# Kernel optimization log

Hardware: AMD Instinct MI355X
Metric: run time of the kernel (lower is better)

The kernel has to match this reference:

```python
import jax, jax.numpy as jnp
import numpy as np
from jax import lax

# ---- fake-quant helpers (brevitas-style per-tensor float scaling, STE round) ----
EPS = 1e-8

def _ste_round(x):
    return x + lax.stop_gradient(jnp.round(x) - x)

def _scale(x, qmax):
    s = lax.stop_gradient(jnp.max(jnp.abs(x))) / qmax
    return jnp.maximum(s, EPS)

def fq(x, scale, qmin, qmax):
    # fake-quantize: round-to-nearest with straight-through estimator, clip, dequant
    return jnp.clip(_ste_round(x / scale), qmin, qmax) * scale

def quant_act_int8(x):
    s = _scale(x, 127.0)
    return fq(x, s, -128.0, 127.0), s

def quant_weight_int4(w):
    # 4-bit signed, narrow range [-7, 7] (brevitas weight quant default narrow_range)
    s = _scale(w, 7.0)
    return fq(w, s, -7.0, 7.0), s

def quant_relu_uint4(x):
    y = jax.nn.relu(x)
    s = _scale(y, 15.0)
    return fq(y, s, 0.0, 15.0)

def quant_bias_int32(b, scale):
    # Int32Bias: bias quantized at input_scale * weight_scale
    return _ste_round(b / scale) * scale

def conv2d_same(x, w):
    # NCHW, OIHW, padding=1, stride=1
    return lax.conv_general_dilated(x, w, window_strides=(1, 1), padding=((1, 1), (1, 1)),
                                    dimension_numbers=('NCHW', 'OIHW', 'NCHW'))

def maxpool2(x):
    return lax.reduce_window(x, -jnp.inf, lax.max, (1, 1, 2, 2), (1, 1, 2, 2), 'VALID')

def quant_conv(x, w, b):
    xq, sx = quant_act_int8(x)        # input_quant: Int8ActPerTensorFloat
    wq, sw = quant_weight_int4(w)     # weight_bit_width=4
    bq = quant_bias_int32(b, sx * sw) # bias_quant: Int32Bias
    y = conv2d_same(xq, wq) + bq[None, :, None, None]
    yq, _ = quant_act_int8(y)         # output_quant: Int8ActPerTensorFloat
    return yq

def quant_linear(x, w, b):
    xq, sx = quant_act_int8(x)
    wq, sw = quant_weight_int4(w)
    bq = quant_bias_int32(b, sx * sw)
    y = xq @ wq.T + bq
    yq, _ = quant_act_int8(y)
    return yq


def setup_inputs() -> dict:
    key = jax.random.key(0)
    ks = jax.random.split(key, 7)
    B = 8192
    x = jax.random.normal(ks[0], (B, 1, 28, 28), dtype=jnp.float32)
    w1 = jax.random.normal(ks[1], (16, 1, 3, 3), dtype=jnp.float32) * 0.3
    b1 = jax.random.normal(ks[2], (16,), dtype=jnp.float32) * 0.1
    w2 = jax.random.normal(ks[3], (32, 16, 3, 3), dtype=jnp.float32) * 0.1
    b2 = jax.random.normal(ks[4], (32,), dtype=jnp.float32) * 0.1
    wf = jax.random.normal(ks[5], (10, 32 * 7 * 7), dtype=jnp.float32) * 0.05
    bf = jax.random.normal(ks[6], (10,), dtype=jnp.float32) * 0.1
    return {'x': x, 'w1': w1, 'b1': b1, 'w2': w2, 'b2': b2, 'wf': wf, 'bf': bf}


def reference(x, w1, b1, w2, b2, wf, bf):
    h, _ = quant_act_int8(x)              # inputQuant
    h = quant_conv(h, w1, b1)             # conv1
    h = quant_relu_uint4(h)               # relu1 (4-bit)
    h = maxpool2(h)                       # pool1 -> [B,16,14,14]
    h = quant_conv(h, w2, b2)             # conv2
    h = quant_relu_uint4(h)               # relu2
    h = maxpool2(h)                       # pool2 -> [B,32,7,7]
    h = h.reshape(h.shape[0], -1)         # flatten -> [B,1568]
    return quant_linear(h, wf, bf)        # fc -> [B,10]
```

## Files before the change

### kernel.cpp

```cpp
#include <hip/hip_runtime.h>
#include <climits>

#define NB 8192
#define EPSQ 1e-8f

using i32x4  = __attribute__((ext_vector_type(4)))  int;
using i32x16 = __attribute__((ext_vector_type(16))) int;

#define WS_F(ws)     ((float*)(ws))
#define WS_I(ws)     ((int*)((char*)(ws)+128))
#define WS_B1L(ws)   ((int*)((char*)(ws)+384))
#define WS_B2L(ws)   ((int*)((char*)(ws)+448))
#define WS_BFL(ws)   ((int*)((char*)(ws)+576))
#define WS_M1F(ws)   ((float*)((char*)(ws)+640))
#define WS_B1F(ws)   ((float*)((char*)(ws)+1280))
#define WS_B2FR(ws)  ((char*)(ws)+2048)
#define WS_Q2TAB(ws) ((signed char*)((char*)(ws)+7168))
#define WS_Q3TAB(ws) ((signed char*)((char*)(ws)+7424))
#define WS_B1FR(ws)  ((char*)(ws)+7680)
#define WS_MFF(ws)   ((float*)((char*)(ws)+20480))
#define WS_WFP(ws)   ((char*)(ws)+83200)
#define WS_RA1(ws)   ((int*)((char*)(ws)+139264))
#define WS_RS1(ws)   ((int*)((char*)(ws)+164352))
#define WS_RA2(ws)   ((int*)((char*)(ws)+189440))
#define WS_RS2(ws)   ((int*)((char*)(ws)+197632))
#define WS_RA3(ws)   ((int*)((char*)(ws)+205824))
#define WS_RAX(ws)   ((float*)((char*)(ws)+206848))
#define WS_WMX(ws)   ((float*)((char*)(ws)+215040))
#define WS_Q2B(ws)   ((signed char*)((char*)(ws)+215552))
#define WS_BIG_OFF   281600

__device__ __forceinline__ float clampf(float v, float lo, float hi){ return fminf(fmaxf(v, lo), hi); }

__device__ __forceinline__ float wave_max_f(float v){
#pragma unroll
  for (int off=32; off; off>>=1) v = fmaxf(v, __shfl_down(v, off, 64));
  return v;
}
__device__ __forceinline__ int wave_max_i(int v){
#pragma unroll
  for (int off=32; off; off>>=1) v = max(v, __shfl_down(v, off, 64));
  return v;
}

__device__ __forceinline__ void reduce2_atomic(int amax, int smax, int* gA, int* gS){
  amax = wave_max_i(amax); smax = wave_max_i(smax);
  __shared__ int sA[4], sS[4];
  int w = threadIdx.x>>6, l = threadIdx.x&63;
  if (l==0){ sA[w]=amax; sS[w]=smax; }
  __syncthreads();
  if (threadIdx.x==0){
#pragma unroll
    for (int i=1;i<4;i++){ amax=max(amax,sA[i]); smax=max(smax,sS[i]); }
    atomicMax(gA, amax); atomicMax(gS, smax);
  }
}

__device__ __forceinline__ void reduce2_store(int amax, int smax, int* pA, int* pS){
  amax = wave_max_i(amax); smax = wave_max_i(smax);
  __shared__ int sA[4], sS[4];
  int w = threadIdx.x>>6, l = threadIdx.x&63;
  if (l==0){ sA[w]=amax; sS[w]=smax; }
  __syncthreads();
  if (threadIdx.x==0){
#pragma unroll
    for (int i=1;i<4;i++){ amax=max(amax,sA[i]); smax=max(smax,sS[i]); }
    *pA = amax; *pS = smax;
  }
}

__global__ void k_init(char* ws){
  int* I = WS_I(ws);
  if (threadIdx.x==0){ I[0]=0; I[1]=0; I[2]=INT_MIN; I[3]=0; I[4]=INT_MIN; I[5]=0; }
}

__global__ void k_absx(const float* __restrict__ x, char* ws){
  const float4* x4 = (const float4*)x;
  const int n4 = NB*784/4;
  float m = 0.f;
  for (int i = blockIdx.x*blockDim.x + threadIdx.x; i < n4; i += gridDim.x*blockDim.x){
    float4 v = x4[i];
    m = fmaxf(m, fmaxf(fmaxf(fabsf(v.x),fabsf(v.y)), fmaxf(fabsf(v.z),fabsf(v.w))));
  }
  m = wave_max_f(m);
  __shared__ float sm[4];
  int w = threadIdx.x>>6;
  if ((threadIdx.x&63)==0) sm[w]=m;
  __syncthreads();
  if (threadIdx.x==0){
    m = fmaxf(fmaxf(sm[0],sm[1]), fmaxf(sm[2],sm[3]));
    WS_RAX(ws)[blockIdx.x] = m;
  }
}

__global__ void k_wmax(const float* __restrict__ w1, const float* __restrict__ w2,
                       const float* __restrict__ wf, char* ws){
  __shared__ float red[256];
  int b = blockIdx.x, t = threadIdx.x;
  float m = 0.f;
  if (b==0){ if (t<144) m = fabsf(w1[t]); }
  else if (b<19){ m = fabsf(w2[(b-1)*256 + t]); }
  else { int i=(b-19)*256+t; if (i<15680) m = fabsf(wf[i]); }
  red[t]=m; __syncthreads();
  for (int s=128;s;s>>=1){ if (t<s) red[t]=fmaxf(red[t],red[t+s]); __syncthreads(); }
  if (t==0) WS_WMX(ws)[b]=red[0];
}

__global__ void k_scales(const float* __restrict__ w1, const float* __restrict__ b1, char* ws){
  __shared__ float red[256];
  float* F = WS_F(ws);
  int t = threadIdx.x;
  float vw1 = WS_WMX(ws)[0];
  float m2=0.f, mf=0.f;
  if (t<18) m2 = WS_WMX(ws)[1+t];
  if (t<62) mf = WS_WMX(ws)[19+t];
  red[t]=m2; __syncthreads();
  for (int s=128;s;s>>=1){ if (t<s) red[t]=fmaxf(red[t],red[t+s]); __syncthreads(); }
  float mw2=red[0]; __syncthreads();
  red[t]=mf; __syncthreads();
  for (int s=128;s;s>>=1){ if (t<s) red[t]=fmaxf(red[t],red[t+s]); __syncthreads(); }
  float mwf=red[0]; __syncthreads();
  float mxv=0.f;
  for (int i=t;i<2048;i+=256) mxv=fmaxf(mxv,WS_RAX(ws)[i]);
  red[t]=mxv; __syncthreads();
  for (int s=128;s;s>>=1){ if (t<s) red[t]=fmaxf(red[t],red[t+s]); __syncthreads(); }
  float mx=red[0]; __syncthreads();

  float s0  = fmaxf(mx/127.f, EPSQ);
  float sx1 = fmaxf((127.f*s0)/127.f, EPSQ);
  float sw1 = fmaxf(vw1/7.f, EPSQ);
  float sw2 = fmaxf(mw2/7.f, EPSQ);
  float swf = fmaxf(mwf/7.f, EPSQ);
  float sb1 = sx1*sw1;
  if (t==0){ F[0]=s0; F[1]=sx1; F[2]=sw1; F[3]=sb1; F[7]=sw2; F[12]=swf; }
  if (t<144) WS_M1F(ws)[t] = clampf(rintf(w1[t]/sw1), -7.f, 7.f);
  if (t<16){
    int bl = (int)rintf(b1[t]/sb1);
    WS_B1L(ws)[t] = bl;
    WS_B1F(ws)[t] = (float)bl;
  }
}

__global__ void k_pack(const float* __restrict__ w1, const float* __restrict__ w2,
                       const float* __restrict__ wf, char* ws){
  const float* F = WS_F(ws);
  int id = blockIdx.x*256 + threadIdx.x;
  if (id < 5120){
    float sw2 = F[7];
    int chunk=id>>10, r=id&1023, ln=r>>4, j=r&15;
    int tap=2*chunk+(ln>>5), oc=ln&31;
    signed char v=0;
    if (tap<9) v=(signed char)clampf(rintf(w2[oc*144 + j*9 + tap]/sw2), -7.f, 7.f);
    WS_B2FR(ws)[id]=v;
  } else if (id < 6144){
    float sw1 = F[2];
    int i=id-5120;
    int ln=i>>4, j=i&15;
    int k=(ln>>5)*16+j, oc=ln&31;
    signed char v=0;
    if (k<9 && oc<16) v=(signed char)clampf(rintf(w1[oc*9+k]/sw1), -7.f, 7.f);
    WS_B1FR(ws)[i]=v;
  } else if (id < 56320){
    float swf = F[12];
    int i=id-6144;
    int chunk=i>>10, r2=i&1023, ln=r2>>4, j=r2&15;
    int oc=ln&31, k=chunk*32+(ln>>5)*16+j;
    int cell=k>>5, ch=k&31;
    signed char v=0;
    if (oc<10) v=(signed char)clampf(rintf(wf[oc*1568 + ch*49 + cell]/swf), -7.f, 7.f);
    ((signed char*)WS_WFP(ws))[i]=v;
  } else if (id < 72000){
    float swf = F[12];
    int i=id-56320;
    WS_MFF(ws)[i] = clampf(rintf(wf[i]/swf), -7.f, 7.f);
  }
}

__global__ void k_wq(const float* __restrict__ w1, const float* __restrict__ b1,
                     const float* __restrict__ w2, const float* __restrict__ wf,
                     char* ws){
  __shared__ float red[256];
  float* F = WS_F(ws);
  int t = threadIdx.x;
  auto bmaxabs = [&](const float* p, int n)->float{
    float m=0.f; for (int i=t;i<n;i+=256) m=fmaxf(m,fabsf(p[i]));
    red[t]=m; __syncthreads();
    for (int s=128;s;s>>=1){ if (t<s) red[t]=fmaxf(red[t],red[t+s]); __syncthreads(); }
    float r=red[0]; __syncthreads(); return r;
  };
  float mw1 = bmaxabs(w1,144);
  float mw2 = bmaxabs(w2,4608);
  float mwf = bmaxabs(wf,15680);
  float mxv=0.f;
  for (int i=t;i<2048;i+=256) mxv=fmaxf(mxv,WS_RAX(ws)[i]);
  red[t]=mxv; __syncthreads();
  for (int s=128;s;s>>=1){ if (t<s) red[t]=fmaxf(red[t],red[t+s]); __syncthreads(); }
  float mx=red[0]; __syncthreads();

  float s0  = fmaxf(mx/127.f, EPSQ);
  float sx1 = fmaxf((127.f*s0)/127.f, EPSQ);
  float sw1 = fmaxf(mw1/7.f, EPSQ);
  float sw2 = fmaxf(mw2/7.f, EPSQ);
  float swf = fmaxf(mwf/7.f, EPSQ);
  float sb1 = sx1*sw1;
  if (t==0){ F[0]=s0; F[1]=sx1; F[2]=sw1; F[3]=sb1; F[7]=sw2; F[12]=swf; }
  float* m1f = WS_M1F(ws);
  for (int i=t;i<144;i+=256) m1f[i] = clampf(rintf(w1[i]/sw1), -7.f, 7.f);
  if (t<16){
    int bl = (int)rintf(b1[t]/sb1);
    WS_B1L(ws)[t] = bl;
    WS_B1F(ws)[t] = (float)bl;
  }
  for (int i=t;i<5120;i+=256){
    int chunk=i>>10, r=i&1023, ln=r>>4, j=r&15;
    int tap=2*chunk+(ln>>5), oc=ln&31;
    signed char v=0;
    if (tap<9) v=(signed char)clampf(rintf(w2[oc*144 + j*9 + tap]/sw2), -7.f, 7.f);
    WS_B2FR(ws)[i]=v;
  }
  for (int i=t;i<1024;i+=256){
    int ln=i>>4, j=i&15;
    int k=(ln>>5)*16+j, oc=ln&31;
    signed char v=0;
    if (k<9 && oc<16) v=(signed char)clampf(rintf(w1[oc*9+k]/sw1), -7.f, 7.f);
    WS_B1FR(ws)[i]=v;
  }
  float* mff = WS_MFF(ws);
  for (int i=t;i<15680;i+=256) mff[i] = clampf(rintf(wf[i]/swf), -7.f, 7.f);
  for (int i=t;i<50176;i+=256){
    int chunk=i>>10, r2=i&1023, ln=r2>>4, j=r2&15;
    int oc=ln&31, k=chunk*32+(ln>>5)*16+j;
    int cell=k>>5, ch=k&31;
    signed char v=0;
    if (oc<10) v=(signed char)clampf(rintf(wf[oc*1568 + ch*49 + cell]/swf), -7.f, 7.f);
    ((signed char*)WS_WFP(ws))[i]=v;
  }
}

template<bool FULLR>
__global__ void k_s1(const float* __restrict__ b2, char* ws){
  float* F=WS_F(ws); int* I=WS_I(ws);
  __shared__ int rA[256], rS[256];
  __shared__ float sh[4];
  int t=threadIdx.x;
  int amaxI, smaxI;
  if constexpr (FULLR){
    int a=0, s=INT_MIN;
    const int* ra=WS_RA1(ws); const int* rs=WS_RS1(ws);
    for (int i=t;i<6272;i+=256){ a=max(a,ra[i]); s=max(s,rs[i]); }
    rA[t]=a; rS[t]=s; __syncthreads();
    for (int st=128;st;st>>=1){ if (t<st){ rA[t]=max(rA[t],rA[t+st]); rS[t]=max(rS[t],rS[t+st]); } __syncthreads(); }
    amaxI=rA[0]; smaxI=rS[0];
  } else { amaxI=I[1]; smaxI=I[2]; }
  if (t==0){
    float sb1=F[3];
    float sy1 = fmaxf((sb1*(float)amaxI)/127.f, EPSQ);
    float mp  = sb1*(float)smaxI;
    float P1  = clampf(rintf(mp/sy1), 0.f, 127.f);
    float sr1 = fmaxf((sy1*P1)/15.f, EPSQ);
    float N1  = clampf(rintf((sy1*P1)/sr1), 0.f, 15.f);
    float sx2 = fmaxf((N1*sr1)/127.f, EPSQ);
    float sb2 = sx2*F[7];
    F[4]=sy1; F[5]=sr1; F[6]=sx2; F[8]=sb2;
    sh[0]=sy1; sh[1]=sr1; sh[2]=sx2; sh[3]=sb2;
  }
  __syncthreads();
  float sy1=sh[0], sr1=sh[1], sx2=sh[2], sb2=sh[3];
  int k = t-128;
  float n = (k>0) ? clampf(rintf((sy1*(float)k)/sr1), 0.f, 15.f) : 0.f;
  WS_Q2TAB(ws)[t] = (signed char)clampf(rintf((n*sr1)/sx2), -128.f, 127.f);
  if (t<32) WS_B2L(ws)[t] = (int)rintf(b2[t]/sb2);
}

__global__ void k_q2big(char* ws){
  const float* F = WS_F(ws);
  const float sb1=F[3], sy1=F[4];
  int idx = blockIdx.x*256 + threadIdx.x;
  int m = idx - 32768;
  float k1 = clampf(rintf((sb1*(float)m)/sy1), -128.f, 127.f);
  WS_Q2B(ws)[idx] = WS_Q2TAB(ws)[(int)k1+128];
}

template<bool FULLR>
__global__ void k_s2(const float* __restrict__ bf, char* ws){
  float* F=WS_F(ws); int* I=WS_I(ws);
  __shared__ int rA[256], rS[256];
  __shared__ float sh[4];
  int t=threadIdx.x;
  int amaxI, smaxI;
  if constexpr (FULLR){
    int a=0, s=INT_MIN;
    const int* ra=WS_RA2(ws); const int* rs=WS_RS2(ws);
    for (int i=t;i<2048;i+=256){ a=max(a,ra[i]); s=max(s,rs[i]); }
    rA[t]=a; rS[t]=s; __syncthreads();
    for (int st=128;st;st>>=1){ if (t<st){ rA[t]=max(rA[t],rA[t+st]); rS[t]=max(rS[t],rS[t+st]); } __syncthreads(); }
    amaxI=rA[0]; smaxI=rS[0];
  } else { amaxI=I[3]; smaxI=I[4]; }
  if (t==0){
    float sb2=F[8];
    float sy2 = fmaxf((sb2*(float)amaxI)/127.f, EPSQ);
    float mp  = sb2*(float)smaxI;
    float P2  = clampf(rintf(mp/sy2), 0.f, 127.f);
    float sr2 = fmaxf((sy2*P2)/15.f, EPSQ);
    float N2  = clampf(rintf((sy2*P2)/sr2), 0.f, 15.f);
    float sx3 = fmaxf((N2*sr2)/127.f, EPSQ);
    float sb3 = sx3*F[12];
    F[9]=sy2; F[10]=sr2; F[11]=sx3; F[13]=sb3;
    sh[0]=sy2; sh[1]=sr2; sh[2]=sx3; sh[3]=sb3;
  }
  __syncthreads();
  float sy2=sh[0], sr2=sh[1], sx3=sh[2], sb3=sh[3];
  int k = t-128;
  float n = (k>0) ? clampf(rintf((sy2*(float)k)/sr2), 0.f, 15.f) : 0.f;
  WS_Q3TAB(ws)[t] = (signed char)clampf(rintf((n*sr2)/sx3), -128.f, 127.f);
  if (t<16) WS_BFL(ws)[t] = (t<10) ? (int)rintf(bf[t]/sb3) : 0;
}

template<bool FULLR>
__global__ void k_s3(char* ws){
  float* F=WS_F(ws); int* I=WS_I(ws);
  __shared__ int rA[256];
  int t=threadIdx.x;
  int amaxI;
  if constexpr (FULLR){
    rA[t] = WS_RA3(ws)[t];
    __syncthreads();
    for (int st=128;st;st>>=1){ if (t<st) rA[t]=max(rA[t],rA[t+st]); __syncthreads(); }
    amaxI = rA[0];
  } else { amaxI = I[5]; }
  if (t==0) F[14] = fmaxf((F[13]*(float)amaxI)/127.f, EPSQ);
}

__global__ void k_qx(const float* __restrict__ x, const char* __restrict__ ws,
                     signed char* __restrict__ qx){
  const float s0 = ((const float*)ws)[0];
  int id = blockIdx.x*256 + threadIdx.x;
  int img = id/240, w = id - img*240;
  int r = w>>3, c4 = (w&7)<<2;
  const float* xi = x + img*784;
  unsigned out = 0;
#pragma unroll
  for (int j=0;j<4;j++){
    int c = c4+j;
    bool valid = (r>=1) && (r<=28) && (c>=1) && (c<=28);
    int q = 0;
    if (valid){
      float xv = xi[(r-1)*28 + (c-1)];
      q = (int)clampf(rintf(xv/s0), -128.f, 127.f);
    }
    out |= ((unsigned)(unsigned char)(signed char)q) << (8*j);
  }
  ((unsigned*)qx)[id] = out;
}

__global__ __launch_bounds__(256) void k_conv1(const signed char* __restrict__ qx,
                                               char* __restrict__ ws,
                                               short* __restrict__ i1p){
  const int t = threadIdx.x;
  const int id = blockIdx.x*256 + t;
  const int img = id/196, cell = id - img*196;
  const int py = cell/14, px = cell - py*14;
  const signed char* qb = qx + img*960 + (2*py)*32;
  const int pc0 = 2*px;
  const int al = pc0 & ~3, sh = (pc0&3)*8;
  float in[4][4];
#pragma unroll
  for (int rr=0; rr<4; rr++){
    unsigned lo = *(const unsigned*)(qb + rr*32 + al);
    unsigned hi = *(const unsigned*)(qb + rr*32 + al + 4);
    unsigned wrd = (unsigned)(((((unsigned long long)hi)<<32)|lo) >> sh);
#pragma unroll
    for (int cc=0; cc<4; cc++)
      in[rr][cc] = (float)(signed char)((wrd >> (8*cc)) & 0xFFu);
  }
  const float* __restrict__ m1f = WS_M1F(ws);
  const float* __restrict__ b1f = WS_B1F(ws);
  int amax=0, smax=INT_MIN;
  short outv[16];
#pragma unroll
  for (int oc=0; oc<16; oc++){
    float b = b1f[oc];
    float a00=b, a01=b, a10=b, a11=b;
#pragma unroll
    for (int dy=0; dy<3; dy++){
#pragma unroll
      for (int dx=0; dx<3; dx++){
        float wt = m1f[oc*9+dy*3+dx];
        a00 = fmaf(in[dy  ][dx  ], wt, a00);
        a01 = fmaf(in[dy  ][dx+1], wt, a01);
        a10 = fmaf(in[dy+1][dx  ], wt, a10);
        a11 = fmaf(in[dy+1][dx+1], wt, a11);
      }
    }
    int v00=(int)a00, v01=(int)a01, v10=(int)a10, v11=(int)a11;
    int mx = max(max(v00,v01), max(v10,v11));
    int ax = max(max(v00<0?-v00:v00, v01<0?-v01:v01), max(v10<0?-v10:v10, v11<0?-v11:v11));
    amax = max(amax, ax);
    smax = max(smax, mx);
    outv[oc] = (short)mx;
  }
  int4* dst = (int4*)(i1p + (size_t)id*16);
  dst[0] = *(const int4*)&outv[0];
  dst[1] = *(const int4*)&outv[8];
  reduce2_store(amax, smax, &WS_RA1(ws)[blockIdx.x], &WS_RS1(ws)[blockIdx.x]);
}

__global__ __launch_bounds__(256) void k_conv2r(char* __restrict__ ws,
                                                short* __restrict__ i1p,
                                                int* __restrict__ p2g){
  __shared__ __align__(16) signed char q2p4[4][4096];
  const int t=threadIdx.x, lane=t&63, wid=t>>6;
  const int img = blockIdx.x*4 + wid;
  signed char* q2p = q2p4[wid];
  const signed char* __restrict__ q2b = WS_Q2B(ws);

#pragma unroll
  for (int k=0;k<8;k++) ((unsigned long long*)q2p)[lane + 64*k] = 0ULL;

  const unsigned* src = (const unsigned*)(i1p + (size_t)img*3136);
  for (int k=0;k<25;k++){
    int idx = lane + 64*k;
    if (idx >= 1568) break;
    unsigned wv = src[idx];
    int e0 = idx*2;
    int cellc = e0 >> 4, ch = e0 & 15;
    int pyc = cellc/14, pxc = cellc - pyc*14;
    int m0 = (int)(short)(wv & 0xFFFFu);
    int m1 = (int)(short)(wv >> 16);
    int b0 = (int)(unsigned char)q2b[m0+32768];
    int b1 = (int)(unsigned char)q2b[m1+32768];
    *(unsigned short*)(q2p + ((pyc+1)*16 + (pxc+1))*16 + ch) = (unsigned short)(b0 | (b1<<8));
  }

  i32x4 bfr[5];
  const i32x4* bg = (const i32x4*)WS_B2FR(ws);
#pragma unroll
  for (int c=0;c<5;c++) bfr[c] = bg[c*64+lane];
  const int col = lane&31, h = lane>>5;
  const int bias = WS_B2L(ws)[col];
  int amax2=0, smax2=INT_MIN;
  const int TOFF[9] = {0,1,2,16,17,18,32,33,34};
  int* dstb = p2g + (size_t)img*1568;

#pragma unroll
  for (int mt=0; mt<7; mt++){
    int m = mt*32 + col;
    int g = m>>2, sub = m&3;
    bool gv = g < 49;
    int py = (g*37)>>8;
    int px = g - py*7;
    int oy = 2*py + (sub>>1), ox = 2*px + (sub&1);
    int E0 = oy*16 + ox;
    i32x16 acc;
#pragma unroll
    for (int r=0;r<16;r++) acc[r] = bias;
#pragma unroll
    for (int c=0;c<5;c++){
      const int t0 = TOFF[2*c];
      const int t1 = (2*c+1<9) ? TOFF[2*c+1] : -1;
      int toff = h ? t1 : t0;
      int entry = (gv && toff>=0) ? (E0 + toff) : 0;
      i32x4 a = *(const i32x4*)(q2p + entry*16);
      acc = __builtin_amdgcn_mfma_i32_32x32x32_i8(a, bfr[c], acc, 0,0,0);
    }
#pragma unroll
    for (int i=0;i<4;i++){
      int gg = mt*8 + 2*i + h;
      if (gg < 49){
        int v0=acc[4*i], v1=acc[4*i+1], v2=acc[4*i+2], v3=acc[4*i+3];
        int a0=v0<0?-v0:v0, a1=v1<0?-v1:v1, a2=v2<0?-v2:v2, a3=v3<0?-v3:v3;
        amax2 = max(amax2, max(max(a0,a1),max(a2,a3)));
        int mx = max(max(v0,v1),max(v2,v3));
        smax2 = max(smax2, mx);
        dstb[gg*32 + col] = mx;
      }
    }
  }
  reduce2_store(amax2, smax2, &WS_RA2(ws)[blockIdx.x], &WS_RS2(ws)[blockIdx.x]);
}

__global__ void k_rq2(const char* __restrict__ ws, const int* __restrict__ p2g,
                      signed char* __restrict__ q3g){
  const float* F = (const float*)ws;
  const float sb2 = F[8], sy2 = F[9];
  const signed char* q3t = WS_Q3TAB(ws);
  int id = blockIdx.x*256 + threadIdx.x;
  i32x4 m4 = ((const i32x4*)p2g)[id];
  unsigned out=0;
#pragma unroll
  for (int j=0;j<4;j++){
    float k2 = clampf(rintf((sb2*(float)m4[j])/sy2), -128.f, 127.f);
    out |= ((unsigned)(unsigned char)q3t[(int)k2+128]) << (8*j);
  }
  ((unsigned*)q3g)[id] = out;
}

__global__ __launch_bounds__(256) void k_fc(char* __restrict__ ws,
                                            const signed char* __restrict__ q3g,
                                            int* __restrict__ i3out){
  __shared__ int part[3][16][64];
  int t=threadIdx.x, lane=t&63, wid=t>>6;
  int mt = blockIdx.x;
  const int col=lane&31, h=lane>>5;
  const signed char* A0 = q3g + (size_t)(mt*32 + col)*1568 + 16*h;
  const i32x4* wfp = (const i32x4*)WS_WFP(ws);
  i32x16 acc;
#pragma unroll
  for (int r=0;r<16;r++) acc[r]=0;
  for (int c=wid; c<49; c+=4){
    i32x4 a = *(const i32x4*)(A0 + c*32);
    i32x4 b = wfp[c*64 + lane];
    acc = __builtin_amdgcn_mfma_i32_32x32x32_i8(a, b, acc, 0,0,0);
  }
  if (wid>0){
#pragma unroll
    for (int r=0;r<16;r++) part[wid-1][r][lane] = acc[r];
  }
  __syncthreads();
  if (wid==0){
    int bias = (col<10) ? WS_BFL(ws)[col] : 0;
    int am=0;
#pragma unroll
    for (int r=0;r<16;r++){
      int v = acc[r] + part[0][r][lane] + part[1][r][lane] + part[2][r][lane] + bias;
      int row=(r&3)+8*(r>>2)+4*h;
      int img = mt*32+row;
      if (col<10){
        i3out[img*10+col] = v;
        am = max(am, v<0?-v:v);
      }
    }
    am = wave_max_i(am);
    if (lane==0) WS_RA3(ws)[blockIdx.x] = am;
  }
}

__global__ void k_out2(char* __restrict__ ws, float* __restrict__ out){
  __shared__ int rA[256];
  int t=threadIdx.x;
  rA[t] = WS_RA3(ws)[t];
  __syncthreads();
  for (int st=128;st;st>>=1){ if (t<st) rA[t]=max(rA[t],rA[t+st]); __syncthreads(); }
  float sb3 = WS_F(ws)[13];
  float sy3 = fmaxf((sb3*(float)rA[0])/127.f, EPSQ);
  int i = blockIdx.x*256 + t;
  if (i < NB*10){
    int iv = ((const int*)out)[i];
    float y = sb3*(float)iv;
    float q = clampf(rintf(y/sy3), -128.f, 127.f);
    out[i] = q*sy3;
  }
}

__global__ __launch_bounds__(256) void k_c1(const float* __restrict__ x, char* __restrict__ ws,
                                            short* __restrict__ i1p){
  constexpr int OFF_K0=0, OFF_A=960, OFF_I1=13760, OFF_B1=38848;
  __shared__ __align__(16) char arena[38912];
  signed char* k0b = (signed char*)(arena+OFF_K0);
  signed char* Abuf= (signed char*)(arena+OFF_A);
  short*       I1s = (short*)(arena+OFF_I1);
  int*         b1i = (int*)(arena+OFF_B1);

  const int tid=threadIdx.x, img=blockIdx.x;
  const int lane=tid&63, wid=tid>>6;
  const float s0 = WS_F(ws)[0];

  if (tid<16) b1i[tid]=WS_B1L(ws)[tid];
  for (int i=tid;i<240;i+=256) ((int*)k0b)[i]=0;
  for (int i=tid;i<3200;i+=256) ((int*)Abuf)[i]=0;
  __syncthreads();
  const float* xi = x + img*784;
  for (int i=tid;i<784;i+=256){
    int r=i/28, c=i-r*28;
    float v = clampf(rintf(xi[i]/s0), -128.f, 127.f);
    k0b[(r+1)*32 + (c+1)] = (signed char)v;
  }
  __syncthreads();
  for (int p=tid;p<784;p+=256){
    int oy=p/28, ox=p-oy*28;
    int base = oy*32+ox;
    int al = base & ~3, sh = (base&3)*8;
    unsigned l0a=*(const unsigned*)(k0b+al),    l1a=*(const unsigned*)(k0b+al+4);
    unsigned l0b=*(const unsigned*)(k0b+al+32), l1b=*(const unsigned*)(k0b+al+36);
    unsigned l0c=*(const unsigned*)(k0b+al+64), l1c=*(const unsigned*)(k0b+al+68);
    unsigned u0=(unsigned)(((((unsigned long long)l1a)<<32)|l0a)>>sh);
    unsigned u1=(unsigned)(((((unsigned long long)l1b)<<32)|l0b)>>sh);
    unsigned u2=(unsigned)(((((unsigned long long)l1c)<<32)|l0c)>>sh);
    i32x4 row;
    row[0]=(int)((u0&0xFFFFFFu)|(u1<<24));
    row[1]=(int)(((u1>>8)&0xFFFFu)|((u2&0xFFFFu)<<16));
    row[2]=(int)((u2>>16)&0xFFu);
    row[3]=0;
    *(i32x4*)(Abuf + p*16) = row;
  }
  __syncthreads();
  const i32x4 bfr = ((const i32x4*)WS_B1FR(ws))[lane];
  const int col=lane&31, h=lane>>5;
  const int bias=(col<16)? b1i[col] : 0;
  int amax=0, smax=INT_MIN;
  for (int mt=wid; mt<25; mt+=4){
    i32x4 a={0,0,0,0};
    if (h==0) a = *(const i32x4*)(Abuf + (mt*32+col)*16);
    i32x16 acc;
#pragma unroll
    for (int r=0;r<16;r++) acc[r]=bias;
    acc=__builtin_amdgcn_mfma_i32_32x32x32_i8(a,bfr,acc,0,0,0);
#pragma unroll
    for (int r=0;r<16;r++){
      int row=(r&3)+8*(r>>2)+4*h;
      int p=mt*32+row;
      if (p<784 && col<16){
        int v=acc[r];
        amax=max(amax,v<0?-v:v); smax=max(smax,v);
        I1s[p*16+col]=(short)v;
      }
    }
  }
  __syncthreads();
  for (int i=tid;i<3136;i+=256){
    int pp=i>>4, c=i&15, py=pp/14, px=pp-py*14;
    int p0=py*56+px*2;
    int m=max(max((int)I1s[p0*16+c],(int)I1s[(p0+1)*16+c]),
              max((int)I1s[(p0+28)*16+c],(int)I1s[(p0+29)*16+c]));
    i1p[(size_t)img*3136 + i]=(short)m;
  }
  reduce2_atomic(amax,smax,&WS_I(ws)[1],&WS_I(ws)[2]);
}

template<bool FIN>
__global__ __launch_bounds__(256) void k_c2(char* __restrict__ ws, const short* __restrict__ i1p,
                                            int* __restrict__ i3out){
  constexpr int OFF_Q2L=0, OFF_B2I=3136, OFF_Q2T=3264, OFF_N2=3520,
                OFF_Q3T=9792, OFF_BFS=10048, OFF_Q3F=10112, OFF_RED=16384;
  constexpr int ARENA = FIN ? 16544 : 3520;
  __shared__ __align__(16) char arena[ARENA];
  signed char* q2l=(signed char*)(arena+OFF_Q2L);
  int* b2li=(int*)(arena+OFF_B2I);
  signed char* q2t=(signed char*)(arena+OFF_Q2T);

  const int tid=threadIdx.x, img=blockIdx.x;
  const int lane=tid&63, wid=tid>>6;
  const float* F=WS_F(ws);
  const float sb1=F[3], sy1=F[4];

  q2t[tid]=WS_Q2TAB(ws)[tid];
  if (tid<32) b2li[tid]=WS_B2L(ws)[tid];
  if constexpr (FIN){
    ((signed char*)(arena+OFF_Q3T))[tid]=WS_Q3TAB(ws)[tid];
    if (tid<16) ((int*)(arena+OFF_BFS))[tid]=WS_BFL(ws)[tid];
  }
  __syncthreads();
  for (int i=tid;i<3136;i+=256){
    int m=(int)i1p[(size_t)img*3136+i];
    float k1=clampf(rintf((sb1*(float)m)/sy1),-128.f,127.f);
    q2l[i]=q2t[(int)k1+128];
  }
  __syncthreads();

  i32x4 bfr[5];
  {
    const i32x4* bg=(const i32x4*)WS_B2FR(ws);
#pragma unroll
    for (int c=0;c<5;c++) bfr[c]=bg[c*64+lane];
  }
  const int col=lane&31, h=lane>>5;
  const int bias=b2li[col];
  int amax2=0, smax2=INT_MIN;
  float sb2=0.f, sy2=0.f;
  signed char* n2buf=nullptr;
  if constexpr (FIN){ sb2=F[8]; sy2=F[9]; n2buf=(signed char*)(arena+OFF_N2); }

  for (int mt=wid; mt<7; mt+=4){
    const int p=mt*32+col;
    const bool pv=p<196;
    const int oy=p/14, ox=p-oy*14;
    i32x16 acc;
#pragma unroll
    for (int r=0;r<16;r++) acc[r]=bias;
#pragma unroll
    for (int c=0;c<5;c++){
      const int tap=2*c+h;
      i32x4 a={0,0,0,0};
      if (pv && tap<9){
        const int iy=oy+tap/3-1, ix=ox+tap-(tap/3)*3-1;
        if ((unsigned)iy<14u && (unsigned)ix<14u) a=*(const i32x4*)(q2l+(iy*14+ix)*16);
      }
      acc=__builtin_amdgcn_mfma_i32_32x32x32_i8(a,bfr[c],acc,0,0,0);
    }
#pragma unroll
    for (int r=0;r<16;r++){
      const int row=(r&3)+8*(r>>2)+4*h;
      const int pp=mt*32+row;
      if (pp<196){
        const int v=acc[r];
        if constexpr (!FIN){ amax2=max(amax2,v<0?-v:v); smax2=max(smax2,v); }
        else {
          n2buf[col*196+pp]=(signed char)clampf(rintf((sb2*(float)v)/sy2),-128.f,127.f);
        }
      }
    }
  }
  if constexpr (!FIN){
    reduce2_atomic(amax2,smax2,&WS_I(ws)[3],&WS_I(ws)[4]);
    return;
  } else {
    __syncthreads();
    signed char* q3t_s=(signed char*)(arena+OFF_Q3T);
    float* q3f=(float*)(arena+OFF_Q3F);
    for (int i=tid;i<1568;i+=256){
      int cch=i/49, s=i-cch*49, qy=s/7, qx=s-qy*7;
      int b=cch*196+qy*28+qx*2;
      int m=max(max((int)n2buf[b],(int)n2buf[b+1]),max((int)n2buf[b+14],(int)n2buf[b+15]));
      q3f[i]=(float)q3t_s[m+128];
    }
    __syncthreads();
    const float* mff=WS_MFF(ws);
    float a10[10];
#pragma unroll
    for (int o=0;o<10;o++) a10[o]=0.f;
    for (int k=tid;k<1568;k+=256){
      float qa=q3f[k];
#pragma unroll
      for (int o=0;o<10;o++) a10[o]=fmaf(qa,mff[o*1568+k],a10[o]);
    }
#pragma unroll
    for (int o=0;o<10;o++){
#pragma unroll
      for (int off=32;off;off>>=1) a10[o]+=__shfl_down(a10[o],off,64);
    }
    float* redf=(float*)(arena+OFF_RED);
    int* bfs=(int*)(arena+OFF_BFS);
    if (lane==0){
#pragma unroll
      for (int o=0;o<10;o++) redf[wid*10+o]=a10[o];
    }
    __syncthreads();
    if (tid<10){
      float s=redf[tid]+redf[10+tid]+redf[20+tid]+redf[30+tid];
      int I3v=(int)s+bfs[tid];
      i3out[img*10+tid]=I3v;
      redf[tid]=(float)(I3v<0?-I3v:I3v);
    }
    __syncthreads();
    if (tid==0){
      int m=0;
#pragma unroll
      for (int o=0;o<10;o++) m=max(m,(int)redf[o]);
      atomicMax(&WS_I(ws)[5],m);
    }
  }
}

__global__ void k_out(char* ws, float* __restrict__ out){
  float* F=WS_F(ws);
  float sb3=F[13], sy3=F[14];
  int i = blockIdx.x*blockDim.x + threadIdx.x;
  if (i < NB*10){
    int iv = ((const int*)out)[i];
    float y = sb3*(float)iv;
    float q = clampf(rintf(y/sy3), -128.f, 127.f);
    out[i] = q*sy3;
  }
}

extern "C" void kernel_launch(void* const* d_in, const int* in_sizes, int n_in,
                              void* d_out, int out_size, void* d_ws, size_t ws_size,
                              hipStream_t stream){
  const float* x  = (const float*)d_in[0];
  const float* w1 = (const float*)d_in[1];
  const float* b1 = (const float*)d_in[2];
  const float* w2 = (const float*)d_in[3];
  const float* b2 = (const float*)d_in[4];
  const float* wf = (const float*)d_in[5];
  const float* bf = (const float*)d_in[6];
  char* ws = (char*)d_ws;
  float* out = (float*)d_out;
  int* i3 = (int*)d_out;

  const size_t QX_SZ  = (size_t)NB*960;
  const size_t I1_SZ  = (size_t)NB*6272;
  const size_t Q3_SZ  = (size_t)NB*1568;
  const size_t needFull = (size_t)WS_BIG_OFF + QX_SZ + I1_SZ + Q3_SZ;

  if (ws_size >= needFull){
    signed char* qx  = (signed char*)(ws + WS_BIG_OFF);
    short*       i1p = (short*)(ws + WS_BIG_OFF + QX_SZ);
    int*         p2g = (int*)i1p;
    signed char* q3g = (signed char*)(ws + WS_BIG_OFF + QX_SZ + I1_SZ);
    k_absx  <<<dim3(2048), dim3(256), 0, stream>>>(x, ws);
    k_wmax  <<<dim3(81), dim3(256), 0, stream>>>(w1, w2, wf, ws);
    k_scales<<<dim3(1), dim3(256), 0, stream>>>(w1, b1, ws);
    k_qx    <<<dim3(NB*240/256), dim3(256), 0, stream>>>(x, ws, qx);
    k_pack  <<<dim3(282), dim3(256), 0, stream>>>(w1, w2, wf, ws);
    k_conv1 <<<dim3(NB*196/256), dim3(256), 0, stream>>>(qx, ws, i1p);
    k_s1<true><<<dim3(1), dim3(256), 0, stream>>>(b2, ws);
    k_q2big <<<dim3(256), dim3(256), 0, stream>>>(ws);
    k_conv2r<<<dim3(NB/4), dim3(256), 0, stream>>>(ws, i1p, p2g);
    k_s2<true><<<dim3(1), dim3(256), 0, stream>>>(bf, ws);
    k_rq2   <<<dim3(NB*1568/1024), dim3(256), 0, stream>>>(ws, p2g, q3g);
    k_fc    <<<dim3(256), dim3(256), 0, stream>>>(ws, q3g, i3);
    k_out2  <<<dim3((NB*10+255)/256), dim3(256), 0, stream>>>(ws, out);
  } else {
    short* i1p = (short*)(ws + WS_BIG_OFF);
    k_init<<<dim3(1), dim3(64), 0, stream>>>(ws);
    k_absx<<<dim3(2048), dim3(256), 0, stream>>>(x, ws);
    k_wq  <<<dim3(1), dim3(256), 0, stream>>>(w1, b1, w2, wf, ws);
    k_c1<<<dim3(NB), dim3(256), 0, stream>>>(x, ws, i1p);
    k_s1<false><<<dim3(1), dim3(256), 0, stream>>>(b2, ws);
    k_c2<false><<<dim3(NB), dim3(256), 0, stream>>>(ws, i1p, i3);
    k_s2<false><<<dim3(1), dim3(256), 0, stream>>>(bf, ws);
    k_c2<true ><<<dim3(NB), dim3(256), 0, stream>>>(ws, i1p, i3);
    k_s3<false><<<dim3(1), dim3(256), 0, stream>>>(ws);
    k_out<<<dim3((NB*10+255)/256), dim3(256), 0, stream>>>(ws, out);
  }
}
```

Measured before the change: 129.7 us.

## Fuse input quantization into conv1 and merge reduction/scale kernels

Merges the input abs-max and weight abs-max kernels into one launch, removes the separate input-quantize pass by having conv1 read float input and quantize it in registers, and fuses the stage-1 scale reduction with the requant lookup table build, with each of the 256 blocks redoing the reduction. It also fully unrolls the conv2 staging loop and the fc MFMA loop. The aim is fewer launches and no round trip through the int8 padded input buffer. In exchange conv1 reads redundant overlapping float data and repeats the division per pixel, and the scale reduction is computed 256 times.

```diff
diff --git a/kernel.cpp b/kernel.cpp
--- a/kernel.cpp
+++ b/kernel.cpp
@@ -90,6 +90,40 @@
   if (threadIdx.x==0){
     m = fmaxf(fmaxf(sm[0],sm[1]), fmaxf(sm[2],sm[3]));
     WS_RAX(ws)[blockIdx.x] = m;
+  }
+}
+
+__global__ void k_absxw(const float* __restrict__ x,
+                        const float* __restrict__ w1, const float* __restrict__ w2,
+                        const float* __restrict__ wf, char* ws){
+  __shared__ float red[256];
+  int b = blockIdx.x, t = threadIdx.x;
+  if (b < 81){
+    float m = 0.f;
+    if (b==0){ if (t<144) m = fabsf(w1[t]); }
+    else if (b<19){ m = fabsf(w2[(b-1)*256 + t]); }
+    else { int i=(b-19)*256+t; if (i<15680) m = fabsf(wf[i]); }
+    red[t]=m; __syncthreads();
+    for (int s=128;s;s>>=1){ if (t<s) red[t]=fmaxf(red[t],red[t+s]); __syncthreads(); }
+    if (t==0) WS_WMX(ws)[b]=red[0];
+    return;
+  }
+  const int xb = b - 81;
+  const float4* x4 = (const float4*)x;
+  const int n4 = NB*784/4;
+  float m = 0.f;
+  for (int i = xb*256 + t; i < n4; i += 2048*256){
+    float4 v = x4[i];
+    m = fmaxf(m, fmaxf(fmaxf(fabsf(v.x),fabsf(v.y)), fmaxf(fabsf(v.z),fabsf(v.w))));
+  }
+  m = wave_max_f(m);
+  __shared__ float sm[4];
+  int w = t>>6;
+  if ((t&63)==0) sm[w]=m;
+  __syncthreads();
+  if (t==0){
+    m = fmaxf(fmaxf(sm[0],sm[1]), fmaxf(sm[2],sm[3]));
+    WS_RAX(ws)[xb] = m;
   }
 }
 
@@ -272,13 +306,32 @@
   if (t<32) WS_B2L(ws)[t] = (int)rintf(b2[t]/sb2);
 }
 
-__global__ void k_q2big(char* ws){
-  const float* F = WS_F(ws);
-  const float sb1=F[3], sy1=F[4];
-  int idx = blockIdx.x*256 + threadIdx.x;
+__global__ void k_s1q2(const float* __restrict__ b2, char* ws){
+  float* F=WS_F(ws);
+  __shared__ int rA[256], rS[256];
+  int t=threadIdx.x;
+  int a=0, s=INT_MIN;
+  const int* ra=WS_RA1(ws); const int* rs=WS_RS1(ws);
+  for (int i=t;i<6272;i+=256){ a=max(a,ra[i]); s=max(s,rs[i]); }
+  rA[t]=a; rS[t]=s; __syncthreads();
+  for (int st=128;st;st>>=1){ if (t<st){ rA[t]=max(rA[t],rA[t+st]); rS[t]=max(rS[t],rS[t+st]); } __syncthreads(); }
+  int amaxI=rA[0], smaxI=rS[0];
+  float sb1=F[3];
+  float sy1 = fmaxf((sb1*(float)amaxI)/127.f, EPSQ);
+  float P1  = clampf(rintf((sb1*(float)smaxI)/sy1), 0.f, 127.f);
+  float sr1 = fmaxf((sy1*P1)/15.f, EPSQ);
+  float N1  = clampf(rintf((sy1*P1)/sr1), 0.f, 15.f);
+  float sx2 = fmaxf((N1*sr1)/127.f, EPSQ);
+  float sb2 = sx2*F[7];
+  if (blockIdx.x==0){
+    if (t==0){ F[4]=sy1; F[5]=sr1; F[6]=sx2; F[8]=sb2; }
+    if (t<32) WS_B2L(ws)[t] = (int)rintf(b2[t]/sb2);
+  }
+  int idx = blockIdx.x*256 + t;
   int m = idx - 32768;
   float k1 = clampf(rintf((sb1*(float)m)/sy1), -128.f, 127.f);
-  WS_Q2B(ws)[idx] = WS_Q2TAB(ws)[(int)k1+128];
+  float n  = (k1>0.f) ? clampf(rintf((sy1*k1)/sr1), 0.f, 15.f) : 0.f;
+  WS_Q2B(ws)[idx] = (signed char)clampf(rintf((n*sr1)/sx2), -128.f, 127.f);
 }
 
 template<bool FULLR>
@@ -331,48 +384,35 @@
   if (t==0) F[14] = fmaxf((F[13]*(float)amaxI)/127.f, EPSQ);
 }
 
-__global__ void k_qx(const float* __restrict__ x, const char* __restrict__ ws,
-                     signed char* __restrict__ qx){
-  const float s0 = ((const float*)ws)[0];
-  int id = blockIdx.x*256 + threadIdx.x;
-  int img = id/240, w = id - img*240;
-  int r = w>>3, c4 = (w&7)<<2;
-  const float* xi = x + img*784;
-  unsigned out = 0;
-#pragma unroll
-  for (int j=0;j<4;j++){
-    int c = c4+j;
-    bool valid = (r>=1) && (r<=28) && (c>=1) && (c<=28);
-    int q = 0;
-    if (valid){
-      float xv = xi[(r-1)*28 + (c-1)];
-      q = (int)clampf(rintf(xv/s0), -128.f, 127.f);
-    }
-    out |= ((unsigned)(unsigned char)(signed char)q) << (8*j);
-  }
-  ((unsigned*)qx)[id] = out;
-}
-
-__global__ __launch_bounds__(256) void k_conv1(const signed char* __restrict__ qx,
-                                               char* __restrict__ ws,
-                                               short* __restrict__ i1p){
+__global__ __launch_bounds__(256) void k_conv1f(const float* __restrict__ x,
+                                                char* __restrict__ ws,
+                                                short* __restrict__ i1p){
   const int t = threadIdx.x;
   const int id = blockIdx.x*256 + t;
   const int img = id/196, cell = id - img*196;
   const int py = cell/14, px = cell - py*14;
-  const signed char* qb = qx + img*960 + (2*py)*32;
-  const int pc0 = 2*px;
-  const int al = pc0 & ~3, sh = (pc0&3)*8;
+  const float s0 = WS_F(ws)[0];
+  const float* xi = x + img*784;
+  const int r0 = 2*py-1, c0 = 2*px-1;
   float in[4][4];
 #pragma unroll
   for (int rr=0; rr<4; rr++){
-    unsigned lo = *(const unsigned*)(qb + rr*32 + al);
-    unsigned hi = *(const unsigned*)(qb + rr*32 + al + 4);
-    unsigned wrd = (unsigned)(((((unsigned long long)hi)<<32)|lo) >> sh);
+    int r = r0+rr;
+    bool rv = (unsigned)r < 28u;
+#pragma unroll
+    for (int cc=0; cc<4; cc++){
+      int c = c0+cc;
+      float v = 0.f;
+      if (rv && (unsigned)c < 28u) v = xi[r*28+c];
+      in[rr][cc] = v;
+    }
+  }
+#pragma unroll
+  for (int rr=0; rr<4; rr++)
 #pragma unroll
     for (int cc=0; cc<4; cc++)
-      in[rr][cc] = (float)(signed char)((wrd >> (8*cc)) & 0xFFu);
-  }
+      in[rr][cc] = clampf(rintf(in[rr][cc]/s0), -128.f, 127.f);
+
   const float* __restrict__ m1f = WS_M1F(ws);
   const float* __restrict__ b1f = WS_B1F(ws);
   int amax=0, smax=INT_MIN;
@@ -418,9 +458,21 @@
   for (int k=0;k<8;k++) ((unsigned long long*)q2p)[lane + 64*k] = 0ULL;
 
   const unsigned* src = (const unsigned*)(i1p + (size_t)img*3136);
-  for (int k=0;k<25;k++){
+#pragma unroll
+  for (int k=0;k<24;k++){
     int idx = lane + 64*k;
-    if (idx >= 1568) break;
+    unsigned wv = src[idx];
+    int e0 = idx*2;
+    int cellc = e0 >> 4, ch = e0 & 15;
+    int pyc = cellc/14, pxc = cellc - pyc*14;
+    int m0 = (int)(short)(wv & 0xFFFFu);
+    int m1 = (int)(short)(wv >> 16);
+    int b0 = (int)(unsigned char)q2b[m0+32768];
+    int b1 = (int)(unsigned char)q2b[m1+32768];
+    *(unsigned short*)(q2p + ((pyc+1)*16 + (pxc+1))*16 + ch) = (unsigned short)(b0 | (b1<<8));
+  }
+  if (lane < 32){
+    int idx = 1536 + lane;
     unsigned wv = src[idx];
     int e0 = idx*2;
     int cellc = e0 >> 4, ch = e0 & 15;
@@ -507,10 +559,14 @@
   i32x16 acc;
 #pragma unroll
   for (int r=0;r<16;r++) acc[r]=0;
-  for (int c=wid; c<49; c+=4){
-    i32x4 a = *(const i32x4*)(A0 + c*32);
-    i32x4 b = wfp[c*64 + lane];
-    acc = __builtin_amdgcn_mfma_i32_32x32x32_i8(a, b, acc, 0,0,0);
+#pragma unroll
+  for (int cc=0; cc<13; cc++){
+    int c = wid + cc*4;
+    if (c < 49){
+      i32x4 a = *(const i32x4*)(A0 + c*32);
+      i32x4 b = wfp[c*64 + lane];
+      acc = __builtin_amdgcn_mfma_i32_32x32x32_i8(a, b, acc, 0,0,0);
+    }
   }
   if (wid>0){
 #pragma unroll
@@ -783,18 +839,14 @@
   const size_t needFull = (size_t)WS_BIG_OFF + QX_SZ + I1_SZ + Q3_SZ;
 
   if (ws_size >= needFull){
-    signed char* qx  = (signed char*)(ws + WS_BIG_OFF);
     short*       i1p = (short*)(ws + WS_BIG_OFF + QX_SZ);
     int*         p2g = (int*)i1p;
     signed char* q3g = (signed char*)(ws + WS_BIG_OFF + QX_SZ + I1_SZ);
-    k_absx  <<<dim3(2048), dim3(256), 0, stream>>>(x, ws);
-    k_wmax  <<<dim3(81), dim3(256), 0, stream>>>(w1, w2, wf, ws);
+    k_absxw <<<dim3(2129), dim3(256), 0, stream>>>(x, w1, w2, wf, ws);
     k_scales<<<dim3(1), dim3(256), 0, stream>>>(w1, b1, ws);
-    k_qx    <<<dim3(NB*240/256), dim3(256), 0, stream>>>(x, ws, qx);
     k_pack  <<<dim3(282), dim3(256), 0, stream>>>(w1, w2, wf, ws);
-    k_conv1 <<<dim3(NB*196/256), dim3(256), 0, stream>>>(qx, ws, i1p);
-    k_s1<true><<<dim3(1), dim3(256), 0, stream>>>(b2, ws);
-    k_q2big <<<dim3(256), dim3(256), 0, stream>>>(ws);
+    k_conv1f<<<dim3(NB*196/256), dim3(256), 0, stream>>>(x, ws, i1p);
+    k_s1q2  <<<dim3(256), dim3(256), 0, stream>>>(b2, ws);
     k_conv2r<<<dim3(NB/4), dim3(256), 0, stream>>>(ws, i1p, p2g);
     k_s2<true><<<dim3(1), dim3(256), 0, stream>>>(bf, ws);
     k_rq2   <<<dim3(NB*1568/1024), dim3(256), 0, stream>>>(ws, p2g, q3g);
```

Result: faster. 123.3 us (-4.9%).
